# Optimization experiments

Hardware: AMD Instinct MI355X
Metric: run time of the kernel (lower is better)

## Reference

```python
import jax, jax.numpy as jnp
import numpy as np

N_NODES = 100000
IN_CH, HIDDEN, OUT_CH = 128, 128, 64
N_POS, N_NEG = 600000, 600000


def _glorot(key, shape):
    lim = float(np.sqrt(6.0 / (shape[0] + shape[1])))
    return jax.random.uniform(key, shape, jnp.float32, -lim, lim)


def setup_inputs() -> dict:
    key = jax.random.key(0)
    k = jax.random.split(key, 7)
    x = jax.random.normal(k[0], (N_NODES, IN_CH), jnp.float32)
    pos_edge_index = jax.random.randint(k[1], (2, N_POS), 0, N_NODES, jnp.int64)
    neg_edge_index = jax.random.randint(k[2], (2, N_NEG), 0, N_NODES, jnp.int64)
    W1 = _glorot(k[3], (IN_CH, HIDDEN))
    b1 = jnp.zeros((HIDDEN,), jnp.float32)
    W2 = _glorot(k[4], (HIDDEN, OUT_CH))
    b2 = jnp.zeros((OUT_CH,), jnp.float32)
    return {"x": x, "pos_edge_index": pos_edge_index, "neg_edge_index": neg_edge_index,
            "W1": W1, "b1": b1, "W2": W2, "b2": b2}


def gcn_conv(x, W, b, src, dst, n_nodes):
    # PyG GCNConv: add self-loops, symmetric deg^-1/2 normalization, linear, bias
    h = x @ W                                               # [N, F_out]
    ones = jnp.ones(src.shape, h.dtype)
    deg = jax.ops.segment_sum(ones, dst, num_segments=n_nodes) + 1.0  # self-loop
    dinv = jax.lax.rsqrt(deg)                               # deg^-0.5, deg >= 1
    norm = dinv[src] * dinv[dst]                            # per-edge norm
    agg = jax.ops.segment_sum(h[src] * norm[:, None], dst, num_segments=n_nodes)
    agg = agg + h * (dinv * dinv)[:, None]                  # self-loop messages
    return agg + b


def reference(x, pos_edge_index, neg_edge_index, W1, b1, W2, b2):
    n = x.shape[0]
    src, dst = pos_edge_index[0], pos_edge_index[1]
    z = gcn_conv(x, W1, b1, src, dst, n)
    z = jax.nn.relu(z)
    z = gcn_conv(z, W2, b2, src, dst, n)
    # decode: gather endpoints of pos+neg edges, elementwise product, sum over feat
    ei = jnp.concatenate([pos_edge_index, neg_edge_index], axis=-1)  # [2, E_pos+E_neg]
    return jnp.sum(z[ei[0]] * z[ei[1]], axis=-1)
```

## Files before the change

### kernel.cpp

```cpp
#include <hip/hip_runtime.h>

#define N_NODES 100000
#define IN_CH 128
#define HIDDEN 128
#define OUT_CH 64
#define N_POS 600000
#define N_NEG 600000

typedef unsigned int uint32;
typedef unsigned short ushort16;
typedef __attribute__((ext_vector_type(8))) short bf16x8;
typedef __attribute__((ext_vector_type(4))) float f32x4;

__device__ inline float bf_lo(uint32 u) {
    union { uint32 i; float f; } v;
    v.i = u << 16;
    return v.f;
}
__device__ inline float bf_hi(uint32 u) {
    union { uint32 i; float f; } v;
    v.i = u & 0xffff0000u;
    return v.f;
}
__device__ inline ushort16 f2bf(float f) {
    union { uint32 i; float f; } v;
    v.f = f;
    uint32 r = v.i + 0x7fffu + ((v.i >> 16) & 1u);
    return (ushort16)(r >> 16);
}
__device__ inline uint32 pack2bf(float a, float b) {
    return (uint32)f2bf(a) | ((uint32)f2bf(b) << 16);
}

#define NB_HIST ((N_POS + 255) / 256)
#define NB_FILL ((N_POS + 255) / 256)
#define NB_GEMM1 ((N_NODES + 63) / 64)

__global__ void hist_wt(const int* __restrict__ dst, int* __restrict__ hist,
                        const float* __restrict__ W1, const float* __restrict__ W2,
                        ushort16* __restrict__ W1t, ushort16* __restrict__ W2t) {
    if (blockIdx.x < NB_HIST) {
        int i = blockIdx.x * 256 + threadIdx.x;
        if (i < N_POS) atomicAdd(&hist[dst[i]], 1);
    } else {
        int i = (blockIdx.x - NB_HIST) * 256 + threadIdx.x;
        if (i < 128 * 128) {
            int n = i >> 7, k = i & 127;
            W1t[i] = f2bf(W1[k * 128 + n]);
        } else {
            int j = i - 128 * 128;
            if (j < 64 * 128) {
                int n = j >> 7, k = j & 127;
                W2t[j] = f2bf(W2[k * 64 + n]);
            }
        }
    }
}

__global__ void scan_reduce(const int* __restrict__ hist, int* __restrict__ partials, int n) {
    __shared__ int sdata[256];
    int b = blockIdx.x, t = threadIdx.x;
    int base = b * 1024;
    int s = 0;
    for (int i = t; i < 1024; i += 256) {
        int idx = base + i;
        s += (idx < n) ? hist[idx] : 0;
    }
    sdata[t] = s;
    __syncthreads();
    for (int off = 128; off > 0; off >>= 1) {
        if (t < off) sdata[t] += sdata[t + off];
        __syncthreads();
    }
    if (t == 0) partials[b] = sdata[0];
}

__global__ void scan_final(const int* __restrict__ hist, const int* __restrict__ partials,
                           int* __restrict__ rowstart, int* __restrict__ cursor,
                           float* __restrict__ dinv, int n) {
    __shared__ int tsum[256];
    __shared__ int base_sh;
    int t = threadIdx.x, b = blockIdx.x;
    if (t < 64) {
        int s0 = (t < b) ? partials[t] : 0;
        int i2 = t + 64;
        int s1 = (i2 < b && i2 < 98) ? partials[i2] : 0;
        int s = s0 + s1;
#pragma unroll
        for (int off = 32; off > 0; off >>= 1) s += __shfl_down(s, off, 64);
        if (t == 0) base_sh = s;
    }
    int base = b * 1024 + t * 4;
    int v[4];
    int s = 0;
#pragma unroll
    for (int j = 0; j < 4; j++) {
        int i = base + j;
        v[j] = (i < n) ? hist[i] : 0;
        s += v[j];
    }
    tsum[t] = s;
    __syncthreads();
    for (int off = 1; off < 256; off <<= 1) {
        int a = (t >= off) ? tsum[t - off] : 0;
        __syncthreads();
        tsum[t] += a;
        __syncthreads();
    }
    int offset = base_sh + (tsum[t] - s);
#pragma unroll
    for (int j = 0; j < 4; j++) {
        int i = base + j;
        if (i < n) {
            rowstart[i] = offset;
            cursor[i] = offset;
            dinv[i] = rsqrtf((float)v[j] + 1.0f);
            offset += v[j];
        }
    }
    if (b == 0 && t == 0) rowstart[n] = N_POS;
}

template <int M, bool XBF>
__device__ __forceinline__ void gemm_tile(const void* __restrict__ Xv,
                                          const ushort16* __restrict__ Wt,
                                          ushort16* __restrict__ H, int n, int tileIdx) {
    constexpr int K = 128;
    constexpr int TN = 64;
    constexpr int XS = 136;
    __shared__ short Xs[TN * XS];
    __shared__ short Ws[M * XS];
    int tid = threadIdx.x;
    int node0 = tileIdx * TN;

    for (int q = tid; q < M * K / 8; q += 256) {
        int row = q >> 4;
        int c = q & 15;
        uint4 v = ((const uint4*)Wt)[q];
        *(uint4*)(Ws + row * XS + c * 8) = v;
    }
    if (!XBF) {
        const float* X = (const float*)Xv;
        int row = tid >> 2, part = tid & 3;
        int gn = node0 + row;
#pragma unroll
        for (int c = 0; c < 8; ++c) {
            int k = part * 32 + c * 4;
            float4 v = (gn < n) ? *(const float4*)(X + (size_t)gn * K + k) : float4{0, 0, 0, 0};
            uint2 p = {pack2bf(v.x, v.y), pack2bf(v.z, v.w)};
            *(uint2*)(Xs + row * XS + k) = p;
        }
    } else {
        const ushort16* X = (const ushort16*)Xv;
        for (int q = tid; q < TN * K / 8; q += 256) {
            int row = q >> 4;
            int c = q & 15;
            int gn = node0 + row;
            uint4 v = (gn < n) ? ((const uint4*)(X + (size_t)gn * K))[c] : uint4{0, 0, 0, 0};
            *(uint4*)(Xs + row * XS + c * 8) = v;
        }
    }
    __syncthreads();

    constexpr int CT = M / 16;
    int w = tid >> 6;
    int lane = tid & 63;
    int l15 = lane & 15;
    int quad = lane >> 4;

    f32x4 acc[CT] = {};
    const short* xrow = Xs + (w * 16 + l15) * XS + quad * 8;
#pragma unroll
    for (int kk = 0; kk < 4; ++kk) {
        bf16x8 a = *(const bf16x8*)(xrow + kk * 32);
#pragma unroll
        for (int ct = 0; ct < CT; ++ct) {
            bf16x8 b = *(const bf16x8*)(Ws + (ct * 16 + l15) * XS + quad * 8 + kk * 32);
            acc[ct] = __builtin_amdgcn_mfma_f32_16x16x32_bf16(a, b, acc[ct], 0, 0, 0);
        }
    }

#pragma unroll
    for (int ct = 0; ct < CT; ++ct) {
#pragma unroll
        for (int r = 0; r < 4; ++r) {
            int gn = node0 + w * 16 + quad * 4 + r;
            if (gn < n) H[(size_t)gn * M + ct * 16 + l15] = f2bf(acc[ct][r]);
        }
    }
}

__global__ __launch_bounds__(256) void csr_gemm1(
    const int* __restrict__ src, const int* __restrict__ dst, const float* __restrict__ dinv,
    int* __restrict__ cursor, int2* __restrict__ adjw, const float* __restrict__ x,
    const ushort16* __restrict__ W1t, ushort16* __restrict__ H, int n) {
    if (blockIdx.x < NB_FILL) {
        int e = blockIdx.x * 256 + threadIdx.x;
        if (e < N_POS) {
            int s = src[e], d = dst[e];
            int p = atomicAdd(&cursor[d], 1);
            adjw[p] = int2{s, __float_as_int(dinv[s] * dinv[d])};
        }
    } else {
        gemm_tile<HIDDEN, false>(x, W1t, H, n, blockIdx.x - NB_FILL);
    }
}

template <int M, bool XBF>
__global__ __launch_bounds__(256) void gemm_mfma(const void* __restrict__ Xv,
                                                 const ushort16* __restrict__ Wt,
                                                 ushort16* __restrict__ H, int n) {
    gemm_tile<M, XBF>(Xv, Wt, H, n, blockIdx.x);
}

template <int F, bool RELU>
__global__ void agg_pull(const int* __restrict__ rowstart, const int2* __restrict__ adjw,
                         const float* __restrict__ dinv, const ushort16* __restrict__ H,
                         const float* __restrict__ bias, ushort16* __restrict__ Z, int n) {
    int g = threadIdx.x >> 4;
    int l = threadIdx.x & 15;
    int node = blockIdx.x * (blockDim.x >> 4) + g;
    if (node >= n) return;
    float dn = dinv[node];
    int rs = rowstart[node], re = rowstart[node + 1];
    int deg = re - rs;
    int pc = (deg > 0) ? rs : (rs > 0 ? rs - 1 : 0);
    if (F == 128) {
        uint4 h[8];
        float wv[8];
#pragma unroll
        for (int j = 0; j < 8; ++j) {
            int p = (rs + j < re) ? rs + j : pc;
            int2 e = adjw[p];
            h[j] = *(const uint4*)(H + (size_t)e.x * F + l * 8);
            wv[j] = (j < deg) ? __int_as_float(e.y) : 0.0f;
        }
        float s0[8] = {}, s1[8] = {};
#pragma unroll
        for (int j = 0; j < 8; j += 2) {
            s0[0] += bf_lo(h[j].x) * wv[j]; s0[1] += bf_hi(h[j].x) * wv[j];
            s0[2] += bf_lo(h[j].y) * wv[j]; s0[3] += bf_hi(h[j].y) * wv[j];
            s0[4] += bf_lo(h[j].z) * wv[j]; s0[5] += bf_hi(h[j].z) * wv[j];
            s0[6] += bf_lo(h[j].w) * wv[j]; s0[7] += bf_hi(h[j].w) * wv[j];
            s1[0] += bf_lo(h[j + 1].x) * wv[j + 1]; s1[1] += bf_hi(h[j + 1].x) * wv[j + 1];
            s1[2] += bf_lo(h[j + 1].y) * wv[j + 1]; s1[3] += bf_hi(h[j + 1].y) * wv[j + 1];
            s1[4] += bf_lo(h[j + 1].z) * wv[j + 1]; s1[5] += bf_hi(h[j + 1].z) * wv[j + 1];
            s1[6] += bf_lo(h[j + 1].w) * wv[j + 1]; s1[7] += bf_hi(h[j + 1].w) * wv[j + 1];
        }
        for (int p = rs + 8; p < re; ++p) {
            int2 e = adjw[p];
            float w = __int_as_float(e.y);
            uint4 hh = *(const uint4*)(H + (size_t)e.x * F + l * 8);
            s0[0] += bf_lo(hh.x) * w; s0[1] += bf_hi(hh.x) * w;
            s0[2] += bf_lo(hh.y) * w; s0[3] += bf_hi(hh.y) * w;
            s0[4] += bf_lo(hh.z) * w; s0[5] += bf_hi(hh.z) * w;
            s0[6] += bf_lo(hh.w) * w; s0[7] += bf_hi(hh.w) * w;
        }
        uint4 hv = *(const uint4*)(H + (size_t)node * F + l * 8);
        float4 bv0 = *(const float4*)(bias + l * 8);
        float4 bv1 = *(const float4*)(bias + l * 8 + 4);
        float d2 = dn * dn;
        float hs[8] = {bf_lo(hv.x), bf_hi(hv.x), bf_lo(hv.y), bf_hi(hv.y),
                       bf_lo(hv.z), bf_hi(hv.z), bf_lo(hv.w), bf_hi(hv.w)};
        float bb[8] = {bv0.x, bv0.y, bv0.z, bv0.w, bv1.x, bv1.y, bv1.z, bv1.w};
        float v[8];
#pragma unroll
        for (int j = 0; j < 8; ++j) {
            v[j] = s0[j] + s1[j] + hs[j] * d2 + bb[j];
            if (RELU) v[j] = fmaxf(v[j], 0.0f);
        }
        *(uint4*)(Z + (size_t)node * F + l * 8) =
            uint4{pack2bf(v[0], v[1]), pack2bf(v[2], v[3]), pack2bf(v[4], v[5]),
                  pack2bf(v[6], v[7])};
    } else {
        uint2 h[8];
        float wv[8];
#pragma unroll
        for (int j = 0; j < 8; ++j) {
            int p = (rs + j < re) ? rs + j : pc;
            int2 e = adjw[p];
            h[j] = *(const uint2*)(H + (size_t)e.x * F + l * 4);
            wv[j] = (j < deg) ? __int_as_float(e.y) : 0.0f;
        }
        float s0[4] = {}, s1[4] = {};
#pragma unroll
        for (int j = 0; j < 8; j += 2) {
            s0[0] += bf_lo(h[j].x) * wv[j]; s0[1] += bf_hi(h[j].x) * wv[j];
            s0[2] += bf_lo(h[j].y) * wv[j]; s0[3] += bf_hi(h[j].y) * wv[j];
            s1[0] += bf_lo(h[j + 1].x) * wv[j + 1]; s1[1] += bf_hi(h[j + 1].x) * wv[j + 1];
            s1[2] += bf_lo(h[j + 1].y) * wv[j + 1]; s1[3] += bf_hi(h[j + 1].y) * wv[j + 1];
        }
        for (int p = rs + 8; p < re; ++p) {
            int2 e = adjw[p];
            float w = __int_as_float(e.y);
            uint2 hh = *(const uint2*)(H + (size_t)e.x * F + l * 4);
            s0[0] += bf_lo(hh.x) * w; s0[1] += bf_hi(hh.x) * w;
            s0[2] += bf_lo(hh.y) * w; s0[3] += bf_hi(hh.y) * w;
        }
        uint2 hv = *(const uint2*)(H + (size_t)node * F + l * 4);
        float4 bv = *(const float4*)(bias + l * 4);
        float d2 = dn * dn;
        float hs[4] = {bf_lo(hv.x), bf_hi(hv.x), bf_lo(hv.y), bf_hi(hv.y)};
        float bb[4] = {bv.x, bv.y, bv.z, bv.w};
        float v[4];
#pragma unroll
        for (int j = 0; j < 4; ++j) {
            v[j] = s0[j] + s1[j] + hs[j] * d2 + bb[j];
            if (RELU) v[j] = fmaxf(v[j], 0.0f);
        }
        *(uint2*)(Z + (size_t)node * F + l * 4) = uint2{pack2bf(v[0], v[1]), pack2bf(v[2], v[3])};
    }
}

__global__ void decode_mfma(const int* __restrict__ pos, const int* __restrict__ neg,
                            const short* __restrict__ Z, float* __restrict__ out) {
    int wid = threadIdx.x >> 6;
    int lane = threadIdx.x & 63;
    int l15 = lane & 15;
    int quad = lane >> 4;
    int e0 = (blockIdx.x * 4 + wid) * 32;
    if (e0 >= N_POS + N_NEG) return;
    const int* bp = (e0 < N_POS) ? pos : (neg - N_POS);
    int eA = e0 + l15;
    int eB = e0 + 16 + l15;
    int aA = bp[eA], bA = bp[600000 + eA];
    int aB = bp[eB], bB = bp[600000 + eB];

    const short* zaA = Z + (size_t)aA * OUT_CH + quad * 8;
    const short* zbA = Z + (size_t)bA * OUT_CH + quad * 8;
    const short* zaB = Z + (size_t)aB * OUT_CH + quad * 8;
    const short* zbB = Z + (size_t)bB * OUT_CH + quad * 8;
    bf16x8 a0A = *(const bf16x8*)(zaA);
    bf16x8 a1A = *(const bf16x8*)(zaA + 32);
    bf16x8 b0A = *(const bf16x8*)(zbA);
    bf16x8 b1A = *(const bf16x8*)(zbA + 32);
    bf16x8 a0B = *(const bf16x8*)(zaB);
    bf16x8 a1B = *(const bf16x8*)(zaB + 32);
    bf16x8 b0B = *(const bf16x8*)(zbB);
    bf16x8 b1B = *(const bf16x8*)(zbB + 32);

    f32x4 accA = {}, accB = {};
    accA = __builtin_amdgcn_mfma_f32_16x16x32_bf16(a0A, b0A, accA, 0, 0, 0);
    accB = __builtin_amdgcn_mfma_f32_16x16x32_bf16(a0B, b0B, accB, 0, 0, 0);
    accA = __builtin_amdgcn_mfma_f32_16x16x32_bf16(a1A, b1A, accA, 0, 0, 0);
    accB = __builtin_amdgcn_mfma_f32_16x16x32_bf16(a1B, b1B, accB, 0, 0, 0);

    if (quad == (l15 >> 2)) {
        out[eA] = accA[l15 & 3];
        out[eB] = accB[l15 & 3];
    }
}

extern "C" void kernel_launch(void* const* d_in, const int* in_sizes, int n_in,
                              void* d_out, int out_size, void* d_ws, size_t ws_size,
                              hipStream_t stream) {
    const float* x = (const float*)d_in[0];
    const int* pos = (const int*)d_in[1];
    const int* neg = (const int*)d_in[2];
    const float* W1 = (const float*)d_in[3];
    const float* b1 = (const float*)d_in[4];
    const float* W2 = (const float*)d_in[5];
    const float* b2 = (const float*)d_in[6];
    float* out = (float*)d_out;

    ushort16* A = (ushort16*)d_ws;
    ushort16* B = A + (size_t)N_NODES * 128;
    float* dinv = (float*)(B + (size_t)N_NODES * 128);
    int* hist = (int*)(dinv + N_NODES);
    int* rowstart = hist + N_NODES;
    int* cursor = rowstart + N_NODES + 1;
    int2* adjw = (int2*)(cursor + N_NODES);
    int* partials = (int*)(adjw + N_POS);
    ushort16* W1t = (ushort16*)(partials + 128);
    ushort16* W2t = W1t + 128 * 128;

    const int* pos_src = pos;
    const int* pos_dst = pos + N_POS;

    constexpr int NB_SCAN = (N_NODES + 1023) / 1024;

    hipMemsetAsync(hist, 0, N_NODES * sizeof(int), stream);
    hist_wt<<<NB_HIST + 96, 256, 0, stream>>>(pos_dst, hist, W1, W2, W1t, W2t);
    scan_reduce<<<NB_SCAN, 256, 0, stream>>>(hist, partials, N_NODES);
    scan_final<<<NB_SCAN, 256, 0, stream>>>(hist, partials, rowstart, cursor, dinv, N_NODES);

    csr_gemm1<<<NB_FILL + NB_GEMM1, 256, 0, stream>>>(pos_src, pos_dst, dinv, cursor, adjw, x,
                                                      W1t, A, N_NODES);

    agg_pull<HIDDEN, true><<<(N_NODES + 15) / 16, 256, 0, stream>>>(rowstart, adjw, dinv, A, b1,
                                                                    B, N_NODES);

    ushort16* h2 = A;
    gemm_mfma<OUT_CH, true><<<(N_NODES + 63) / 64, 256, 0, stream>>>(B, W2t, h2, N_NODES);
    ushort16* z2 = B;
    agg_pull<OUT_CH, false><<<(N_NODES + 15) / 16, 256, 0, stream>>>(rowstart, adjw, dinv, h2, b2,
                                                                     z2, N_NODES);

    decode_mfma<<<(N_POS + N_NEG) / 128, 256, 0, stream>>>(pos, neg, (const short*)z2, out);
}
```

Before: 275.6 us.

## Store CSR adjacency as source ids only and read GEMM weights from global

The CSR fill now writes only the source index per edge instead of an int2 holding the precomputed edge weight. The aggregation kernels recompute the weight as dinv[src]*dinv[node], which halves adjacency traffic at the cost of an extra gather into dinv. Separately, the GEMM tile no longer stages the transposed weight matrix in shared memory; each lane loads B fragments straight from global (L2-resident) memory and preloads its A fragments into registers. This cuts LDS usage and a staging pass but relies on cache hits for the repeated weight loads.

```diff
diff --git a/kernel.cpp b/kernel.cpp
--- a/kernel.cpp
+++ b/kernel.cpp
@@ -129,16 +129,9 @@
     constexpr int TN = 64;
     constexpr int XS = 136;
     __shared__ short Xs[TN * XS];
-    __shared__ short Ws[M * XS];
     int tid = threadIdx.x;
     int node0 = tileIdx * TN;
 
-    for (int q = tid; q < M * K / 8; q += 256) {
-        int row = q >> 4;
-        int c = q & 15;
-        uint4 v = ((const uint4*)Wt)[q];
-        *(uint4*)(Ws + row * XS + c * 8) = v;
-    }
     if (!XBF) {
         const float* X = (const float*)Xv;
         int row = tid >> 2, part = tid & 3;
@@ -170,13 +163,17 @@
 
     f32x4 acc[CT] = {};
     const short* xrow = Xs + (w * 16 + l15) * XS + quad * 8;
+    bf16x8 a[4];
+#pragma unroll
+    for (int kk = 0; kk < 4; ++kk) a[kk] = *(const bf16x8*)(xrow + kk * 32);
+
+    const short* wrow = (const short*)Wt + l15 * K + quad * 8;
 #pragma unroll
     for (int kk = 0; kk < 4; ++kk) {
-        bf16x8 a = *(const bf16x8*)(xrow + kk * 32);
 #pragma unroll
         for (int ct = 0; ct < CT; ++ct) {
-            bf16x8 b = *(const bf16x8*)(Ws + (ct * 16 + l15) * XS + quad * 8 + kk * 32);
-            acc[ct] = __builtin_amdgcn_mfma_f32_16x16x32_bf16(a, b, acc[ct], 0, 0, 0);
+            bf16x8 b = *(const bf16x8*)(wrow + ct * 16 * K + kk * 32);
+            acc[ct] = __builtin_amdgcn_mfma_f32_16x16x32_bf16(a[kk], b, acc[ct], 0, 0, 0);
         }
     }
 
@@ -191,15 +188,15 @@
 }
 
 __global__ __launch_bounds__(256) void csr_gemm1(
-    const int* __restrict__ src, const int* __restrict__ dst, const float* __restrict__ dinv,
-    int* __restrict__ cursor, int2* __restrict__ adjw, const float* __restrict__ x,
-    const ushort16* __restrict__ W1t, ushort16* __restrict__ H, int n) {
+    const int* __restrict__ src, const int* __restrict__ dst, int* __restrict__ cursor,
+    int* __restrict__ adj, const float* __restrict__ x, const ushort16* __restrict__ W1t,
+    ushort16* __restrict__ H, int n) {
     if (blockIdx.x < NB_FILL) {
         int e = blockIdx.x * 256 + threadIdx.x;
         if (e < N_POS) {
             int s = src[e], d = dst[e];
             int p = atomicAdd(&cursor[d], 1);
-            adjw[p] = int2{s, __float_as_int(dinv[s] * dinv[d])};
+            adj[p] = s;
         }
     } else {
         gemm_tile<HIDDEN, false>(x, W1t, H, n, blockIdx.x - NB_FILL);
@@ -214,7 +211,7 @@
 }
 
 template <int F, bool RELU>
-__global__ void agg_pull(const int* __restrict__ rowstart, const int2* __restrict__ adjw,
+__global__ void agg_pull(const int* __restrict__ rowstart, const int* __restrict__ adj,
                          const float* __restrict__ dinv, const ushort16* __restrict__ H,
                          const float* __restrict__ bias, ushort16* __restrict__ Z, int n) {
     int g = threadIdx.x >> 4;
@@ -231,9 +228,9 @@
 #pragma unroll
         for (int j = 0; j < 8; ++j) {
             int p = (rs + j < re) ? rs + j : pc;
-            int2 e = adjw[p];
-            h[j] = *(const uint4*)(H + (size_t)e.x * F + l * 8);
-            wv[j] = (j < deg) ? __int_as_float(e.y) : 0.0f;
+            int s = adj[p];
+            h[j] = *(const uint4*)(H + (size_t)s * F + l * 8);
+            wv[j] = (j < deg) ? dinv[s] * dn : 0.0f;
         }
         float s0[8] = {}, s1[8] = {};
 #pragma unroll
@@ -248,9 +245,9 @@
             s1[6] += bf_lo(h[j + 1].w) * wv[j + 1]; s1[7] += bf_hi(h[j + 1].w) * wv[j + 1];
         }
         for (int p = rs + 8; p < re; ++p) {
-            int2 e = adjw[p];
-            float w = __int_as_float(e.y);
-            uint4 hh = *(const uint4*)(H + (size_t)e.x * F + l * 8);
+            int s = adj[p];
+            float w = dinv[s] * dn;
+            uint4 hh = *(const uint4*)(H + (size_t)s * F + l * 8);
             s0[0] += bf_lo(hh.x) * w; s0[1] += bf_hi(hh.x) * w;
             s0[2] += bf_lo(hh.y) * w; s0[3] += bf_hi(hh.y) * w;
             s0[4] += bf_lo(hh.z) * w; s0[5] += bf_hi(hh.z) * w;
@@ -278,9 +275,9 @@
 #pragma unroll
         for (int j = 0; j < 8; ++j) {
             int p = (rs + j < re) ? rs + j : pc;
-            int2 e = adjw[p];
-            h[j] = *(const uint2*)(H + (size_t)e.x * F + l * 4);
-            wv[j] = (j < deg) ? __int_as_float(e.y) : 0.0f;
+            int s = adj[p];
+            h[j] = *(const uint2*)(H + (size_t)s * F + l * 4);
+            wv[j] = (j < deg) ? dinv[s] * dn : 0.0f;
         }
         float s0[4] = {}, s1[4] = {};
 #pragma unroll
@@ -291,9 +288,9 @@
             s1[2] += bf_lo(h[j + 1].y) * wv[j + 1]; s1[3] += bf_hi(h[j + 1].y) * wv[j + 1];
         }
         for (int p = rs + 8; p < re; ++p) {
-            int2 e = adjw[p];
-            float w = __int_as_float(e.y);
-            uint2 hh = *(const uint2*)(H + (size_t)e.x * F + l * 4);
+            int s = adj[p];
+            float w = dinv[s] * dn;
+            uint2 hh = *(const uint2*)(H + (size_t)s * F + l * 4);
             s0[0] += bf_lo(hh.x) * w; s0[1] += bf_hi(hh.x) * w;
             s0[2] += bf_lo(hh.y) * w; s0[3] += bf_hi(hh.y) * w;
         }
@@ -369,8 +366,8 @@
     int* hist = (int*)(dinv + N_NODES);
     int* rowstart = hist + N_NODES;
     int* cursor = rowstart + N_NODES + 1;
-    int2* adjw = (int2*)(cursor + N_NODES);
-    int* partials = (int*)(adjw + N_POS);
+    int* adj = cursor + N_NODES;
+    int* partials = adj + N_POS;
     ushort16* W1t = (ushort16*)(partials + 128);
     ushort16* W2t = W1t + 128 * 128;
 
@@ -384,16 +381,16 @@
     scan_reduce<<<NB_SCAN, 256, 0, stream>>>(hist, partials, N_NODES);
     scan_final<<<NB_SCAN, 256, 0, stream>>>(hist, partials, rowstart, cursor, dinv, N_NODES);
 
-    csr_gemm1<<<NB_FILL + NB_GEMM1, 256, 0, stream>>>(pos_src, pos_dst, dinv, cursor, adjw, x,
-                                                      W1t, A, N_NODES);
-
-    agg_pull<HIDDEN, true><<<(N_NODES + 15) / 16, 256, 0, stream>>>(rowstart, adjw, dinv, A, b1,
-                                                                    B, N_NODES);
+    csr_gemm1<<<NB_FILL + NB_GEMM1, 256, 0, stream>>>(pos_src, pos_dst, cursor, adj, x, W1t, A,
+                                                      N_NODES);
+
+    agg_pull<HIDDEN, true><<<(N_NODES + 15) / 16, 256, 0, stream>>>(rowstart, adj, dinv, A, b1, B,
+                                                                    N_NODES);
 
     ushort16* h2 = A;
     gemm_mfma<OUT_CH, true><<<(N_NODES + 63) / 64, 256, 0, stream>>>(B, W2t, h2, N_NODES);
     ushort16* z2 = B;
-    agg_pull<OUT_CH, false><<<(N_NODES + 15) / 16, 256, 0, stream>>>(rowstart, adjw, dinv, h2, b2,
+    agg_pull<OUT_CH, false><<<(N_NODES + 15) / 16, 256, 0, stream>>>(rowstart, adj, dinv, h2, b2,
                                                                      z2, N_NODES);
 
     decode_mfma<<<(N_POS + N_NEG) / 128, 256, 0, stream>>>(pos, neg, (const short*)z2, out);
```

After: 333.6 us. 1.21x slower.
